# Optimization experiments

Hardware: AMD Instinct MI355X
Metric: run time of the kernel (lower is better)

## Reference

```python
import jax, jax.numpy as jnp
import numpy as np

DIM = 512
NUM_HEADS = 8
HEAD_DIM = DIM // NUM_HEADS


def setup_inputs() -> dict:
    key = jax.random.key(0)
    k1, k2, k3, k4 = jax.random.split(key, 4)
    B, N = 8, 32 * 32
    x = jax.random.normal(k1, (B, N, DIM), dtype=jnp.float32)
    # nn.Linear(dim, 3*dim, bias=False): weight [3*dim, dim], y = x @ W.T
    w_qkv = jax.random.normal(k2, (3 * DIM, DIM), dtype=jnp.float32) * 0.02
    w_proj = jax.random.normal(k3, (DIM, DIM), dtype=jnp.float32) * 0.02
    log_decay = jnp.zeros((NUM_HEADS,), dtype=jnp.float32)
    return {"x": x, "w_qkv": w_qkv, "w_proj": w_proj, "log_decay": log_decay,
            "H": 32, "W": 32}


def _manhattan_dist(H: int, W: int) -> jnp.ndarray:
    # [H*W, H*W] Manhattan distance between grid positions
    rows = jnp.repeat(jnp.arange(H), W)  # [N]
    cols = jnp.tile(jnp.arange(W), H)    # [N]
    dist = (jnp.abs(rows[:, None] - rows[None, :])
            + jnp.abs(cols[:, None] - cols[None, :]))
    return dist.astype(jnp.float32)


def reference(x, w_qkv, w_proj, log_decay, H, W):
    B, N, C = x.shape
    nh, hd = NUM_HEADS, HEAD_DIM
    scale = hd ** -0.5
    qkv = jnp.einsum('bnc,dc->bnd', x, w_qkv)          # [B, N, 3C]
    qkv = qkv.reshape(B, N, 3, nh, hd).transpose(2, 0, 3, 1, 4)
    q, k, v = qkv[0], qkv[1], qkv[2]                   # [B, nh, N, hd]
    attn = jnp.einsum('bhid,bhjd->bhij', q, k) * scale  # [B, nh, N, N]
    dist = _manhattan_dist(H, W)                        # [N, N]
    decay = jax.nn.softplus(log_decay)                  # [nh]
    bias = -decay[:, None, None] * dist[None]           # [nh, N, N]
    attn = jax.nn.softmax(attn + bias[None], axis=-1)
    out = jnp.einsum('bhij,bhjd->bhid', attn, v)        # [B, nh, N, hd]
    out = out.transpose(0, 2, 1, 3).reshape(B, N, C)
    return jnp.einsum('bnc,dc->bnd', out, w_proj)


if __name__ == "__main__":
    out = reference(**setup_inputs())
    print(out.shape, out.dtype)
```

## Files before the change

### kernel.cpp

```cpp
#include <hip/hip_runtime.h>
#include <stdint.h>

typedef _Float16 f16;
typedef _Float16 f16x8 __attribute__((ext_vector_type(8)));
typedef _Float16 f16x4 __attribute__((ext_vector_type(4)));
typedef _Float16 f16x2 __attribute__((ext_vector_type(2)));
typedef float f32x4 __attribute__((ext_vector_type(4)));

#define MROWS 8192
#define KDIM 512
#define NSEQ 1024
#define NH 8

__device__ __forceinline__ void gload16(void* lds, const void* g) {
  __builtin_amdgcn_global_load_lds(
      (const __attribute__((address_space(1))) unsigned*)g,
      (__attribute__((address_space(3))) unsigned*)lds, 16, 0, 0);
}

__device__ __forceinline__ f32x4 mfma16(f16x8 a, f16x8 b, f32x4 c) {
  return __builtin_amdgcn_mfma_f32_16x16x32_f16(a, b, c, 0, 0, 0);
}

__global__ __launch_bounds__(256) void cvt_kernel(
    const float* __restrict__ x, const float* __restrict__ wq,
    const float* __restrict__ wp, f16* __restrict__ x16,
    f16* __restrict__ wq16, f16* __restrict__ wp16) {
  int t = blockIdx.x * 256 + threadIdx.x;
  int stride = gridDim.x * 256;
  for (int i = t; i < (MROWS * KDIM) / 4; i += stride) {
    float4 v = ((const float4*)x)[i];
    f16x4 o = {(f16)v.x, (f16)v.y, (f16)v.z, (f16)v.w};
    ((f16x4*)x16)[i] = o;
  }
  for (int i = t; i < (3 * KDIM * KDIM) / 4; i += stride) {
    float4 v = ((const float4*)wq)[i];
    f16x4 o = {(f16)v.x, (f16)v.y, (f16)v.z, (f16)v.w};
    ((f16x4*)wq16)[i] = o;
  }
  for (int i = t; i < (KDIM * KDIM) / 4; i += stride) {
    float4 v = ((const float4*)wp)[i];
    f16x4 o = {(f16)v.x, (f16)v.y, (f16)v.z, (f16)v.w};
    ((f16x4*)wp16)[i] = o;
  }
}

__device__ __forceinline__ void gemm_mainloop_db(
    const f16* __restrict__ A, const f16* __restrict__ B, int m0, int n0,
    f16* As0, f16* As1, f16* Bs0, f16* Bs1, f32x4 (&acc)[4][4]) {
  const int tid = threadIdx.x;
  const int w = tid >> 6, l = tid & 63;
  const int wr = w >> 1, wc = w & 1;
  const int lrow = l & 15, lk = l >> 4;
  const int srow = l >> 3, sslot = l & 7;
  const int scol = ((sslot ^ srow) << 3);
  const int NT = KDIM / 64;

  auto STAGE = [&](int bb, int kb) {
    f16* Ad = bb ? As1 : As0;
    f16* Bd = bb ? Bs1 : Bs0;
#pragma unroll
    for (int j = 0; j < 4; ++j) {
      int i = w * 4 + j;
      int row = i * 8 + srow;
      gload16(Ad + i * 512, A + (size_t)(m0 + row) * KDIM + kb + scol);
      gload16(Bd + i * 512, B + (size_t)(n0 + row) * KDIM + kb + scol);
    }
  };

  STAGE(0, 0);
#pragma unroll 1
  for (int t = 0; t < NT; ++t) {
    if (t + 1 < NT) {
      STAGE((t + 1) & 1, (t + 1) * 64);
      asm volatile("s_waitcnt vmcnt(8)" ::: "memory");
    } else {
      asm volatile("s_waitcnt vmcnt(0)" ::: "memory");
    }
    __builtin_amdgcn_s_barrier();
    const f16* Asr = (t & 1) ? As1 : As0;
    const f16* Bsr = (t & 1) ? Bs1 : Bs0;
#pragma unroll
    for (int kk = 0; kk < 2; ++kk) {
      int slotbase = kk * 4 + lk;
      f16x8 af[4], bf[4];
#pragma unroll
      for (int mi = 0; mi < 4; ++mi) {
        int row = wr * 64 + mi * 16 + lrow;
        af[mi] = *(const f16x8*)(Asr + row * 64 + ((slotbase ^ (row & 7)) << 3));
      }
#pragma unroll
      for (int nj = 0; nj < 4; ++nj) {
        int row = wc * 64 + nj * 16 + lrow;
        bf[nj] = *(const f16x8*)(Bsr + row * 64 + ((slotbase ^ (row & 7)) << 3));
      }
#pragma unroll
      for (int mi = 0; mi < 4; ++mi)
#pragma unroll
        for (int nj = 0; nj < 4; ++nj)
          acc[mi][nj] = mfma16(af[mi], bf[nj], acc[mi][nj]);
    }
    __builtin_amdgcn_s_barrier();
  }
}

__global__ __launch_bounds__(256, 2) void qkv_gemm(
    const f16* __restrict__ x16, const f16* __restrict__ wq16,
    f16* __restrict__ q16, f16* __restrict__ k16, f16* __restrict__ v16) {
  __shared__ f16 As0[128 * 64], As1[128 * 64];
  __shared__ f16 Bs0[128 * 64], Bs1[128 * 64];
  f32x4 acc[4][4];
#pragma unroll
  for (int i = 0; i < 4; ++i)
#pragma unroll
    for (int j = 0; j < 4; ++j) acc[i][j] = (f32x4){0.f, 0.f, 0.f, 0.f};

  const int m0 = blockIdx.y * 128, n0 = blockIdx.x * 128;
  gemm_mainloop_db(x16, wq16, m0, n0, As0, As1, Bs0, Bs1, acc);

  const int tid = threadIdx.x;
  const int w = tid >> 6, l = tid & 63;
  const int wr = w >> 1, wc = w & 1;
#pragma unroll
  for (int mi = 0; mi < 4; ++mi) {
#pragma unroll
    for (int rr = 0; rr < 4; ++rr) {
      int m = m0 + wr * 64 + mi * 16 + (l >> 4) * 4 + rr;
      int b = m >> 10, n = m & 1023;
#pragma unroll
      for (int nj = 0; nj < 4; ++nj) {
        int d = n0 + wc * 64 + nj * 16 + (l & 15);
        int which = d >> 9, c = d & 511;
        int h = c >> 6, dd = c & 63;
        f16* dst = (which == 0) ? q16 : (which == 1) ? k16 : v16;
        dst[(((size_t)(b * NH + h)) * NSEQ + n) * 64 + dd] = (f16)acc[mi][nj][rr];
      }
    }
  }
}

__global__ __launch_bounds__(256, 2) void proj_gemm(
    const f16* __restrict__ a16, const f16* __restrict__ wp16,
    float* __restrict__ out) {
  __shared__ f16 As0[128 * 64], As1[128 * 64];
  __shared__ f16 Bs0[128 * 64], Bs1[128 * 64];
  f32x4 acc[4][4];
#pragma unroll
  for (int i = 0; i < 4; ++i)
#pragma unroll
    for (int j = 0; j < 4; ++j) acc[i][j] = (f32x4){0.f, 0.f, 0.f, 0.f};

  const int m0 = blockIdx.y * 128, n0 = blockIdx.x * 128;
  gemm_mainloop_db(a16, wp16, m0, n0, As0, As1, Bs0, Bs1, acc);

  const int tid = threadIdx.x;
  const int w = tid >> 6, l = tid & 63;
  const int wr = w >> 1, wc = w & 1;
#pragma unroll
  for (int mi = 0; mi < 4; ++mi) {
#pragma unroll
    for (int rr = 0; rr < 4; ++rr) {
      int m = m0 + wr * 64 + mi * 16 + (l >> 4) * 4 + rr;
#pragma unroll
      for (int nj = 0; nj < 4; ++nj) {
        int d = n0 + wc * 64 + nj * 16 + (l & 15);
        out[(size_t)m * KDIM + d] = acc[mi][nj][rr];
      }
    }
  }
}

__device__ __forceinline__ int swzd(int d) {
  return ((d >> 1) & 3) | ((d & 1) << 2);
}

__global__ __launch_bounds__(256, 2) void attn_f16(
    const f16* __restrict__ q16, const f16* __restrict__ k16,
    const f16* __restrict__ v16, const float* __restrict__ log_decay,
    f16* __restrict__ aout) {
  __shared__ f16 Ks0[64 * 64], Ks1[64 * 64];
  __shared__ f16 Vs0[64 * 64], Vs1[64 * 64];
  __shared__ f16 Vt[64 * 64];
  __shared__ f16 Ps[128 * 64];

  const int tid = threadIdx.x;
  const int w = tid >> 6, l = tid & 63;
  const int lrow = l & 15, lk = l >> 4;
  const int srow = l >> 3, sslot = l & 7;
  const int scol = ((sslot ^ srow) << 3);
  const int q0 = blockIdx.x * 128;
  const int h = blockIdx.y, b = blockIdx.z;
  const size_t base = ((size_t)(b * NH + h)) * NSEQ * 64;

  const float decay = log1pf(__expf(log_decay[h]));

  f16x8 qf[2][2];
#pragma unroll
  for (int njq = 0; njq < 2; ++njq)
#pragma unroll
    for (int kk = 0; kk < 2; ++kk) {
      int row = q0 + w * 32 + njq * 16 + lrow;
      f16x8 v = *(const f16x8*)(q16 + base + (size_t)row * 64 + kk * 32 + lk * 8);
#pragma unroll
      for (int e = 0; e < 8; ++e) v[e] = v[e] * (f16)0.125f;
      qf[njq][kk] = v;
    }

  int qr_[2], qc_[2];
#pragma unroll
  for (int njq = 0; njq < 2; ++njq) {
    int qn = q0 + w * 32 + njq * 16 + lrow;
    qr_[njq] = qn >> 5;
    qc_[njq] = qn & 31;
  }

  f32x4 O[2][4];
#pragma unroll
  for (int njq = 0; njq < 2; ++njq)
#pragma unroll
    for (int dj = 0; dj < 4; ++dj) O[njq][dj] = (f32x4){0.f, 0.f, 0.f, 0.f};
  float mrow[2] = {-1e30f, -1e30f}, lsum[2] = {0.f, 0.f};

  auto STAGE_T = [&](int bb, int c0) {
    f16* Kd = bb ? Ks1 : Ks0;
    f16* Vd = bb ? Vs1 : Vs0;
#pragma unroll
    for (int j = 0; j < 2; ++j) {
      int i = w * 2 + j;
      int row = i * 8 + srow;
      gload16(Kd + i * 512, k16 + base + (size_t)(c0 + row) * 64 + scol);
      gload16(Vd + i * 512, v16 + base + (size_t)(c0 + row) * 64 + (sslot << 3));
    }
  };

  STAGE_T(0, 0);
#pragma unroll 1
  for (int t = 0; t < NSEQ / 64; ++t) {
    const int c0 = t * 64;
    const int cur = t & 1;
    if (t + 1 < NSEQ / 64) {
      STAGE_T(cur ^ 1, c0 + 64);
      asm volatile("s_waitcnt vmcnt(4)" ::: "memory");
    } else {
      asm volatile("s_waitcnt vmcnt(0)" ::: "memory");
    }
    __builtin_amdgcn_s_barrier();

    {
      const f16* vsrc = cur ? Vs1 : Vs0;
      int dd = (tid & 31) * 2;
      int kq = tid >> 5;
      f16x8 v0, v1;
#pragma unroll
      for (int i = 0; i < 8; ++i) {
        f16x2 pr = *(const f16x2*)(vsrc + (size_t)(kq * 8 + i) * 64 + dd);
        v0[i] = pr.x;
        v1[i] = pr.y;
      }
      *(f16x8*)(Vt + (size_t)dd * 64 + ((kq ^ swzd(dd)) << 3)) = v0;
      *(f16x8*)(Vt + (size_t)(dd + 1) * 64 + ((kq ^ swzd(dd + 1)) << 3)) = v1;
    }

    const f16* ksrc = cur ? Ks1 : Ks0;
    f32x4 s[4][2];
#pragma unroll
    for (int mi = 0; mi < 4; ++mi)
#pragma unroll
      for (int njq = 0; njq < 2; ++njq) s[mi][njq] = (f32x4){0.f, 0.f, 0.f, 0.f};
#pragma unroll
    for (int kk = 0; kk < 2; ++kk) {
      int slotbase = kk * 4 + lk;
#pragma unroll
      for (int mi = 0; mi < 4; ++mi) {
        int row = mi * 16 + lrow;
        f16x8 kf = *(const f16x8*)(ksrc + row * 64 + ((slotbase ^ (row & 7)) << 3));
#pragma unroll
        for (int njq = 0; njq < 2; ++njq)
          s[mi][njq] = mfma16(kf, qf[njq][kk], s[mi][njq]);
      }
    }

    float al[2];
#pragma unroll
    for (int njq = 0; njq < 2; ++njq) {
      float mx = -1e30f;
#pragma unroll
      for (int mi = 0; mi < 4; ++mi) {
        int kvb = c0 + mi * 16 + lk * 4;
        int krb = kvb >> 5, kcb = kvb & 31;
        float dr = (float)__builtin_abs(qr_[njq] - krb);
        int t1 = qc_[njq] - kcb;
#pragma unroll
        for (int rr = 0; rr < 4; ++rr) {
          float dc = (float)__builtin_abs(t1 - rr);
          float tt = fmaf(-decay, dr + dc, s[mi][njq][rr]);
          s[mi][njq][rr] = tt;
          mx = fmaxf(mx, tt);
        }
      }
      mx = fmaxf(mx, __shfl_xor(mx, 16));
      mx = fmaxf(mx, __shfl_xor(mx, 32));
      float mnew = fmaxf(mrow[njq], mx);
      al[njq] = __expf(mrow[njq] - mnew);
      mrow[njq] = mnew;
      float rs = 0.f;
      int qq = w * 32 + njq * 16 + lrow;
#pragma unroll
      for (int mi = 0; mi < 4; ++mi) {
        f16x4 pw;
#pragma unroll
        for (int rr = 0; rr < 4; ++rr) {
          float p = __expf(s[mi][njq][rr] - mnew);
          rs += p;
          pw[rr] = (f16)p;
        }
        int slot = mi * 2 + (lk >> 1);
        *(f16x4*)(Ps + qq * 64 + ((slot ^ (qq & 7)) << 3) + ((lk & 1) << 2)) = pw;
      }
      rs += __shfl_xor(rs, 16);
      rs += __shfl_xor(rs, 32);
      lsum[njq] = lsum[njq] * al[njq] + rs;
    }

#pragma unroll
    for (int njq = 0; njq < 2; ++njq) {
#pragma unroll
      for (int rr = 0; rr < 4; ++rr) {
        float a = __shfl(al[njq], lk * 4 + rr);
#pragma unroll
        for (int dj = 0; dj < 4; ++dj) O[njq][dj][rr] *= a;
      }
    }

    asm volatile("s_waitcnt lgkmcnt(0)" ::: "memory");
    __builtin_amdgcn_s_barrier();

#pragma unroll
    for (int kk = 0; kk < 2; ++kk) {
      int slotbase = kk * 4 + lk;
      f16x8 pa[2], vb[4];
#pragma unroll
      for (int njq = 0; njq < 2; ++njq) {
        int row = w * 32 + njq * 16 + lrow;
        pa[njq] = *(const f16x8*)(Ps + row * 64 + ((slotbase ^ (row & 7)) << 3));
      }
#pragma unroll
      for (int dj = 0; dj < 4; ++dj) {
        int d = dj * 16 + lrow;
        vb[dj] = *(const f16x8*)(Vt + d * 64 + ((slotbase ^ swzd(d)) << 3));
      }
#pragma unroll
      for (int njq = 0; njq < 2; ++njq)
#pragma unroll
        for (int dj = 0; dj < 4; ++dj)
          O[njq][dj] = mfma16(pa[njq], vb[dj], O[njq][dj]);
    }
  }

  float linv[2] = {1.f / lsum[0], 1.f / lsum[1]};
#pragma unroll
  for (int njq = 0; njq < 2; ++njq) {
#pragma unroll
    for (int rr = 0; rr < 4; ++rr) {
      float inv = __shfl(linv[njq], lk * 4 + rr);
      int qn = q0 + w * 32 + njq * 16 + lk * 4 + rr;
      size_t rowbase = ((size_t)(b * NSEQ + qn)) * KDIM + h * 64;
#pragma unroll
      for (int dj = 0; dj < 4; ++dj)
        aout[rowbase + dj * 16 + lrow] = (f16)(O[njq][dj][rr] * inv);
    }
  }
}

extern "C" void kernel_launch(void* const* d_in, const int* in_sizes, int n_in,
                              void* d_out, int out_size, void* d_ws, size_t ws_size,
                              hipStream_t stream) {
  const float* x = (const float*)d_in[0];
  const float* w_qkv = (const float*)d_in[1];
  const float* w_proj = (const float*)d_in[2];
  const float* log_decay = (const float*)d_in[3];

  f16* ws = (f16*)d_ws;
  f16* x16 = ws;
  f16* wq16 = x16 + (size_t)MROWS * KDIM;
  f16* wp16 = wq16 + (size_t)3 * KDIM * KDIM;
  f16* q16 = wp16 + (size_t)KDIM * KDIM;
  f16* k16 = q16 + (size_t)MROWS * KDIM;
  f16* v16 = k16 + (size_t)MROWS * KDIM;
  f16* a16 = v16 + (size_t)MROWS * KDIM;

  cvt_kernel<<<1024, 256, 0, stream>>>(x, w_qkv, w_proj, x16, wq16, wp16);
  qkv_gemm<<<dim3(12, 64), 256, 0, stream>>>(x16, wq16, q16, k16, v16);
  attn_f16<<<dim3(8, NH, 8), 256, 0, stream>>>(q16, k16, v16, log_decay, a16);
  proj_gemm<<<dim3(4, 64), 256, 0, stream>>>(a16, wp16, (float*)d_out);
}
```

Before: 155.8 us.

## Store V transposed from QKV GEMM and pass P through registers in attention

The QKV GEMM now writes V in a transposed [head, dim, seq] layout, so the attention kernel loads V tiles straight into LDS already transposed and no longer transposes them per tile. Softmax probabilities are packed to f16 and redistributed into the MFMA A-operand layout with cross-lane shuffles instead of going through an LDS P buffer. The attention block tile shrinks to 64 queries (one 16-row slice per wave) and the grid doubles, with launch bounds raised to 4 blocks per CU. The goals are less LDS traffic, fewer barriers and higher occupancy. The cost is strided scalar stores of V in the GEMM epilogue and extra shuffle instructions per tile.

```diff
diff --git a/kernel.cpp b/kernel.cpp
--- a/kernel.cpp
+++ b/kernel.cpp
@@ -20,6 +20,10 @@
 
 __device__ __forceinline__ f32x4 mfma16(f16x8 a, f16x8 b, f32x4 c) {
   return __builtin_amdgcn_mfma_f32_16x16x32_f16(a, b, c, 0, 0, 0);
+}
+
+__device__ __forceinline__ int vsg(int d) {
+  return ((d >> 1) & 7) ^ ((d & 1) << 2);
 }
 
 __global__ __launch_bounds__(256) void cvt_kernel(
@@ -106,7 +110,7 @@
 
 __global__ __launch_bounds__(256, 2) void qkv_gemm(
     const f16* __restrict__ x16, const f16* __restrict__ wq16,
-    f16* __restrict__ q16, f16* __restrict__ k16, f16* __restrict__ v16) {
+    f16* __restrict__ q16, f16* __restrict__ k16, f16* __restrict__ v16T) {
   __shared__ f16 As0[128 * 64], As1[128 * 64];
   __shared__ f16 Bs0[128 * 64], Bs1[128 * 64];
   f32x4 acc[4][4];
@@ -132,8 +136,14 @@
         int d = n0 + wc * 64 + nj * 16 + (l & 15);
         int which = d >> 9, c = d & 511;
         int h = c >> 6, dd = c & 63;
-        f16* dst = (which == 0) ? q16 : (which == 1) ? k16 : v16;
-        dst[(((size_t)(b * NH + h)) * NSEQ + n) * 64 + dd] = (f16)acc[mi][nj][rr];
+        f16 val = (f16)acc[mi][nj][rr];
+        size_t hb = (size_t)(b * NH + h);
+        if (which == 0)
+          q16[(hb * NSEQ + n) * 64 + dd] = val;
+        else if (which == 1)
+          k16[(hb * NSEQ + n) * 64 + dd] = val;
+        else
+          v16T[(hb * 64 + dd) * NSEQ + n] = val;
       }
     }
   }
@@ -170,205 +180,173 @@
   }
 }
 
-__device__ __forceinline__ int swzd(int d) {
-  return ((d >> 1) & 3) | ((d & 1) << 2);
-}
-
-__global__ __launch_bounds__(256, 2) void attn_f16(
+__global__ __launch_bounds__(256, 4) void attn_f16(
     const f16* __restrict__ q16, const f16* __restrict__ k16,
-    const f16* __restrict__ v16, const float* __restrict__ log_decay,
+    const f16* __restrict__ v16T, const float* __restrict__ log_decay,
     f16* __restrict__ aout) {
   __shared__ f16 Ks0[64 * 64], Ks1[64 * 64];
-  __shared__ f16 Vs0[64 * 64], Vs1[64 * 64];
-  __shared__ f16 Vt[64 * 64];
-  __shared__ f16 Ps[128 * 64];
+  __shared__ f16 Vt0[64 * 64], Vt1[64 * 64];
 
   const int tid = threadIdx.x;
   const int w = tid >> 6, l = tid & 63;
   const int lrow = l & 15, lk = l >> 4;
   const int srow = l >> 3, sslot = l & 7;
-  const int scol = ((sslot ^ srow) << 3);
-  const int q0 = blockIdx.x * 128;
+  const int q0 = blockIdx.x * 64;
   const int h = blockIdx.y, b = blockIdx.z;
-  const size_t base = ((size_t)(b * NH + h)) * NSEQ * 64;
+  const size_t kbase = ((size_t)(b * NH + h)) * NSEQ * 64;
+  const size_t vbase = ((size_t)(b * NH + h)) * 64 * NSEQ;
 
   const float decay = log1pf(__expf(log_decay[h]));
 
-  f16x8 qf[2][2];
-#pragma unroll
-  for (int njq = 0; njq < 2; ++njq)
-#pragma unroll
-    for (int kk = 0; kk < 2; ++kk) {
-      int row = q0 + w * 32 + njq * 16 + lrow;
-      f16x8 v = *(const f16x8*)(q16 + base + (size_t)row * 64 + kk * 32 + lk * 8);
-#pragma unroll
-      for (int e = 0; e < 8; ++e) v[e] = v[e] * (f16)0.125f;
-      qf[njq][kk] = v;
-    }
-
-  int qr_[2], qc_[2];
-#pragma unroll
-  for (int njq = 0; njq < 2; ++njq) {
-    int qn = q0 + w * 32 + njq * 16 + lrow;
-    qr_[njq] = qn >> 5;
-    qc_[njq] = qn & 31;
-  }
-
-  f32x4 O[2][4];
-#pragma unroll
-  for (int njq = 0; njq < 2; ++njq)
-#pragma unroll
-    for (int dj = 0; dj < 4; ++dj) O[njq][dj] = (f32x4){0.f, 0.f, 0.f, 0.f};
-  float mrow[2] = {-1e30f, -1e30f}, lsum[2] = {0.f, 0.f};
-
-  auto STAGE_T = [&](int bb, int c0) {
+  f16x8 qf[2];
+#pragma unroll
+  for (int kk = 0; kk < 2; ++kk) {
+    int row = q0 + w * 16 + lrow;
+    f16x8 v = *(const f16x8*)(q16 + kbase + (size_t)row * 64 + kk * 32 + lk * 8);
+#pragma unroll
+    for (int e = 0; e < 8; ++e) v[e] = v[e] * (f16)0.125f;
+    qf[kk] = v;
+  }
+
+  const int qn = q0 + w * 16 + lrow;
+  const int qr = qn >> 5, qc = qn & 31;
+
+  f32x4 O[4];
+#pragma unroll
+  for (int dj = 0; dj < 4; ++dj) O[dj] = (f32x4){0.f, 0.f, 0.f, 0.f};
+  float mrow = -1e30f, lsum = 0.f;
+
+  auto STAGE = [&](int bb, int c0) {
     f16* Kd = bb ? Ks1 : Ks0;
-    f16* Vd = bb ? Vs1 : Vs0;
+    f16* Vd = bb ? Vt1 : Vt0;
 #pragma unroll
     for (int j = 0; j < 2; ++j) {
       int i = w * 2 + j;
-      int row = i * 8 + srow;
-      gload16(Kd + i * 512, k16 + base + (size_t)(c0 + row) * 64 + scol);
-      gload16(Vd + i * 512, v16 + base + (size_t)(c0 + row) * 64 + (sslot << 3));
+      int krow = i * 8 + srow;
+      gload16(Kd + i * 512,
+              k16 + kbase + (size_t)(c0 + krow) * 64 + ((sslot ^ (krow & 7)) << 3));
+      int d = i * 8 + srow;
+      gload16(Vd + i * 512,
+              v16T + vbase + (size_t)d * NSEQ + c0 + ((sslot ^ vsg(d)) << 3));
     }
   };
 
-  STAGE_T(0, 0);
+  const int srcA = lrow + ((l >> 4) & 1) * 32;
+  const int srcB = srcA + 16;
+  const int msel = lk >> 1;
+
+  STAGE(0, 0);
 #pragma unroll 1
   for (int t = 0; t < NSEQ / 64; ++t) {
     const int c0 = t * 64;
     const int cur = t & 1;
+    __builtin_amdgcn_s_barrier();
     if (t + 1 < NSEQ / 64) {
-      STAGE_T(cur ^ 1, c0 + 64);
+      STAGE(cur ^ 1, c0 + 64);
       asm volatile("s_waitcnt vmcnt(4)" ::: "memory");
     } else {
       asm volatile("s_waitcnt vmcnt(0)" ::: "memory");
     }
     __builtin_amdgcn_s_barrier();
-
-    {
-      const f16* vsrc = cur ? Vs1 : Vs0;
-      int dd = (tid & 31) * 2;
-      int kq = tid >> 5;
-      f16x8 v0, v1;
-#pragma unroll
-      for (int i = 0; i < 8; ++i) {
-        f16x2 pr = *(const f16x2*)(vsrc + (size_t)(kq * 8 + i) * 64 + dd);
-        v0[i] = pr.x;
-        v1[i] = pr.y;
-      }
-      *(f16x8*)(Vt + (size_t)dd * 64 + ((kq ^ swzd(dd)) << 3)) = v0;
-      *(f16x8*)(Vt + (size_t)(dd + 1) * 64 + ((kq ^ swzd(dd + 1)) << 3)) = v1;
-    }
-
-    const f16* ksrc = cur ? Ks1 : Ks0;
-    f32x4 s[4][2];
-#pragma unroll
-    for (int mi = 0; mi < 4; ++mi)
-#pragma unroll
-      for (int njq = 0; njq < 2; ++njq) s[mi][njq] = (f32x4){0.f, 0.f, 0.f, 0.f};
+    const f16* Kc = cur ? Ks1 : Ks0;
+    const f16* Vc = cur ? Vt1 : Vt0;
+
+    f32x4 s[4];
+#pragma unroll
+    for (int mi = 0; mi < 4; ++mi) s[mi] = (f32x4){0.f, 0.f, 0.f, 0.f};
 #pragma unroll
     for (int kk = 0; kk < 2; ++kk) {
-      int slotbase = kk * 4 + lk;
 #pragma unroll
       for (int mi = 0; mi < 4; ++mi) {
         int row = mi * 16 + lrow;
-        f16x8 kf = *(const f16x8*)(ksrc + row * 64 + ((slotbase ^ (row & 7)) << 3));
-#pragma unroll
-        for (int njq = 0; njq < 2; ++njq)
-          s[mi][njq] = mfma16(kf, qf[njq][kk], s[mi][njq]);
-      }
-    }
-
-    float al[2];
-#pragma unroll
-    for (int njq = 0; njq < 2; ++njq) {
-      float mx = -1e30f;
-#pragma unroll
-      for (int mi = 0; mi < 4; ++mi) {
-        int kvb = c0 + mi * 16 + lk * 4;
-        int krb = kvb >> 5, kcb = kvb & 31;
-        float dr = (float)__builtin_abs(qr_[njq] - krb);
-        int t1 = qc_[njq] - kcb;
-#pragma unroll
-        for (int rr = 0; rr < 4; ++rr) {
-          float dc = (float)__builtin_abs(t1 - rr);
-          float tt = fmaf(-decay, dr + dc, s[mi][njq][rr]);
-          s[mi][njq][rr] = tt;
-          mx = fmaxf(mx, tt);
-        }
-      }
-      mx = fmaxf(mx, __shfl_xor(mx, 16));
-      mx = fmaxf(mx, __shfl_xor(mx, 32));
-      float mnew = fmaxf(mrow[njq], mx);
-      al[njq] = __expf(mrow[njq] - mnew);
-      mrow[njq] = mnew;
-      float rs = 0.f;
-      int qq = w * 32 + njq * 16 + lrow;
-#pragma unroll
-      for (int mi = 0; mi < 4; ++mi) {
-        f16x4 pw;
-#pragma unroll
-        for (int rr = 0; rr < 4; ++rr) {
-          float p = __expf(s[mi][njq][rr] - mnew);
-          rs += p;
-          pw[rr] = (f16)p;
-        }
-        int slot = mi * 2 + (lk >> 1);
-        *(f16x4*)(Ps + qq * 64 + ((slot ^ (qq & 7)) << 3) + ((lk & 1) << 2)) = pw;
-      }
-      rs += __shfl_xor(rs, 16);
-      rs += __shfl_xor(rs, 32);
-      lsum[njq] = lsum[njq] * al[njq] + rs;
-    }
-
-#pragma unroll
-    for (int njq = 0; njq < 2; ++njq) {
+        f16x8 kf = *(const f16x8*)(Kc + row * 64 + (((kk * 4 + lk) ^ (row & 7)) << 3));
+        s[mi] = mfma16(kf, qf[kk], s[mi]);
+      }
+    }
+
+    float mx = -1e30f;
+#pragma unroll
+    for (int mi = 0; mi < 4; ++mi) {
+      int kvb = c0 + mi * 16 + lk * 4;
+      int krb = kvb >> 5, kcb = kvb & 31;
+      float dr = (float)__builtin_abs(qr - krb);
+      int t1 = qc - kcb;
 #pragma unroll
       for (int rr = 0; rr < 4; ++rr) {
-        float a = __shfl(al[njq], lk * 4 + rr);
-#pragma unroll
-        for (int dj = 0; dj < 4; ++dj) O[njq][dj][rr] *= a;
-      }
-    }
-
-    asm volatile("s_waitcnt lgkmcnt(0)" ::: "memory");
-    __builtin_amdgcn_s_barrier();
+        float dc = (float)__builtin_abs(t1 - rr);
+        float tt = fmaf(-decay, dr + dc, s[mi][rr]);
+        s[mi][rr] = tt;
+        mx = fmaxf(mx, tt);
+      }
+    }
+    mx = fmaxf(mx, __shfl_xor(mx, 16));
+    mx = fmaxf(mx, __shfl_xor(mx, 32));
+    float mnew = fmaxf(mrow, mx);
+    float al = __expf(mrow - mnew);
+    mrow = mnew;
+    float rs = 0.f;
+    unsigned wpk[4][2];
+#pragma unroll
+    for (int mi = 0; mi < 4; ++mi) {
+#pragma unroll
+      for (int j = 0; j < 2; ++j) {
+        float p0 = __expf(s[mi][2 * j] - mnew);
+        float p1 = __expf(s[mi][2 * j + 1] - mnew);
+        rs += p0 + p1;
+        union { f16x2 h; unsigned u; } pk;
+        pk.h = (f16x2){(f16)p0, (f16)p1};
+        wpk[mi][j] = pk.u;
+      }
+    }
+    rs += __shfl_xor(rs, 16);
+    rs += __shfl_xor(rs, 32);
+    lsum = lsum * al + rs;
+
+#pragma unroll
+    for (int rr = 0; rr < 4; ++rr) {
+      float a = __shfl(al, lk * 4 + rr);
+#pragma unroll
+      for (int dj = 0; dj < 4; ++dj) O[dj][rr] *= a;
+    }
 
 #pragma unroll
     for (int kk = 0; kk < 2; ++kk) {
-      int slotbase = kk * 4 + lk;
-      f16x8 pa[2], vb[4];
-#pragma unroll
-      for (int njq = 0; njq < 2; ++njq) {
-        int row = w * 32 + njq * 16 + lrow;
-        pa[njq] = *(const f16x8*)(Ps + row * 64 + ((slotbase ^ (row & 7)) << 3));
-      }
+      unsigned paw[4];
+      {
+        int a0 = __shfl((int)wpk[kk * 2][0], srcA);
+        int b0 = __shfl((int)wpk[kk * 2 + 1][0], srcA);
+        paw[0] = (unsigned)(msel ? b0 : a0);
+        int a1 = __shfl((int)wpk[kk * 2][1], srcA);
+        int b1 = __shfl((int)wpk[kk * 2 + 1][1], srcA);
+        paw[1] = (unsigned)(msel ? b1 : a1);
+        int a2 = __shfl((int)wpk[kk * 2][0], srcB);
+        int b2 = __shfl((int)wpk[kk * 2 + 1][0], srcB);
+        paw[2] = (unsigned)(msel ? b2 : a2);
+        int a3 = __shfl((int)wpk[kk * 2][1], srcB);
+        int b3 = __shfl((int)wpk[kk * 2 + 1][1], srcB);
+        paw[3] = (unsigned)(msel ? b3 : a3);
+      }
+      union { unsigned u[4]; f16x8 v; } pc;
+      pc.u[0] = paw[0]; pc.u[1] = paw[1]; pc.u[2] = paw[2]; pc.u[3] = paw[3];
+      f16x8 pa = pc.v;
 #pragma unroll
       for (int dj = 0; dj < 4; ++dj) {
         int d = dj * 16 + lrow;
-        vb[dj] = *(const f16x8*)(Vt + d * 64 + ((slotbase ^ swzd(d)) << 3));
-      }
-#pragma unroll
-      for (int njq = 0; njq < 2; ++njq)
-#pragma unroll
-        for (int dj = 0; dj < 4; ++dj)
-          O[njq][dj] = mfma16(pa[njq], vb[dj], O[njq][dj]);
-    }
-  }
-
-  float linv[2] = {1.f / lsum[0], 1.f / lsum[1]};
-#pragma unroll
-  for (int njq = 0; njq < 2; ++njq) {
-#pragma unroll
-    for (int rr = 0; rr < 4; ++rr) {
-      float inv = __shfl(linv[njq], lk * 4 + rr);
-      int qn = q0 + w * 32 + njq * 16 + lk * 4 + rr;
-      size_t rowbase = ((size_t)(b * NSEQ + qn)) * KDIM + h * 64;
-#pragma unroll
-      for (int dj = 0; dj < 4; ++dj)
-        aout[rowbase + dj * 16 + lrow] = (f16)(O[njq][dj][rr] * inv);
-    }
+        f16x8 vb = *(const f16x8*)(Vc + d * 64 + (((kk * 4 + lk) ^ vsg(d)) << 3));
+        O[dj] = mfma16(pa, vb, O[dj]);
+      }
+    }
+  }
+
+  float linv = 1.f / lsum;
+#pragma unroll
+  for (int rr = 0; rr < 4; ++rr) {
+    float inv = __shfl(linv, lk * 4 + rr);
+    int q = q0 + w * 16 + lk * 4 + rr;
+    size_t rowbase = ((size_t)(b * NSEQ + q)) * KDIM + h * 64;
+#pragma unroll
+    for (int dj = 0; dj < 4; ++dj)
+      aout[rowbase + dj * 16 + lrow] = (f16)(O[dj][rr] * inv);
   }
 }
 
@@ -386,11 +364,11 @@
   f16* wp16 = wq16 + (size_t)3 * KDIM * KDIM;
   f16* q16 = wp16 + (size_t)KDIM * KDIM;
   f16* k16 = q16 + (size_t)MROWS * KDIM;
-  f16* v16 = k16 + (size_t)MROWS * KDIM;
-  f16* a16 = v16 + (size_t)MROWS * KDIM;
+  f16* v16T = k16 + (size_t)MROWS * KDIM;
+  f16* a16 = v16T + (size_t)MROWS * KDIM;
 
   cvt_kernel<<<1024, 256, 0, stream>>>(x, w_qkv, w_proj, x16, wq16, wp16);
-  qkv_gemm<<<dim3(12, 64), 256, 0, stream>>>(x16, wq16, q16, k16, v16);
-  attn_f16<<<dim3(8, NH, 8), 256, 0, stream>>>(q16, k16, v16, log_decay, a16);
+  qkv_gemm<<<dim3(12, 64), 256, 0, stream>>>(x16, wq16, q16, k16, v16T);
+  attn_f16<<<dim3(16, NH, 8), 256, 0, stream>>>(q16, k16, v16T, log_decay, a16);
   proj_gemm<<<dim3(4, 64), 256, 0, stream>>>(a16, wp16, (float*)d_out);
 }
```

Result: slower. 172.9 us (+10.9%).

## Emit V transposed from QKV GEMM and double-buffer P in attention

Applied to the files above, without the earlier changes.

The QKV GEMM epilogue now writes V in a head-dim-major transposed layout, staged through shared memory so the stores are coalesced. The attention kernel can then load V^T straight into swizzled LDS instead of transposing it in every tile. Attention also double-buffers the P tile, precomputes the column part of the Manhattan bias per lane, and remaps the grid so blocks for the same (batch, head) are spread out. The prefetch moves to after the barrier and waits vmcnt(0), which may expose more load latency in exchange for removing the per-tile transpose and a barrier hazard.

```diff
diff --git a/kernel.cpp b/kernel.cpp
--- a/kernel.cpp
+++ b/kernel.cpp
@@ -4,7 +4,6 @@
 typedef _Float16 f16;
 typedef _Float16 f16x8 __attribute__((ext_vector_type(8)));
 typedef _Float16 f16x4 __attribute__((ext_vector_type(4)));
-typedef _Float16 f16x2 __attribute__((ext_vector_type(2)));
 typedef float f32x4 __attribute__((ext_vector_type(4)));
 
 #define MROWS 8192
@@ -20,6 +19,10 @@
 
 __device__ __forceinline__ f32x4 mfma16(f16x8 a, f16x8 b, f32x4 c) {
   return __builtin_amdgcn_mfma_f32_16x16x32_f16(a, b, c, 0, 0, 0);
+}
+
+__device__ __forceinline__ int vsg(int d) {
+  return ((d >> 1) & 7) ^ ((d & 1) << 2);
 }
 
 __global__ __launch_bounds__(256) void cvt_kernel(
@@ -106,9 +109,13 @@
 
 __global__ __launch_bounds__(256, 2) void qkv_gemm(
     const f16* __restrict__ x16, const f16* __restrict__ wq16,
-    f16* __restrict__ q16, f16* __restrict__ k16, f16* __restrict__ v16) {
-  __shared__ f16 As0[128 * 64], As1[128 * 64];
-  __shared__ f16 Bs0[128 * 64], Bs1[128 * 64];
+    f16* __restrict__ q16, f16* __restrict__ k16, f16* __restrict__ v16T) {
+  __shared__ f16 SMEM[4 * 128 * 64];
+  f16* As0 = SMEM;
+  f16* As1 = SMEM + 8192;
+  f16* Bs0 = SMEM + 16384;
+  f16* Bs1 = SMEM + 24576;
+
   f32x4 acc[4][4];
 #pragma unroll
   for (int i = 0; i < 4; ++i)
@@ -121,20 +128,54 @@
   const int tid = threadIdx.x;
   const int w = tid >> 6, l = tid & 63;
   const int wr = w >> 1, wc = w & 1;
-#pragma unroll
-  for (int mi = 0; mi < 4; ++mi) {
-#pragma unroll
-    for (int rr = 0; rr < 4; ++rr) {
-      int m = m0 + wr * 64 + mi * 16 + (l >> 4) * 4 + rr;
-      int b = m >> 10, n = m & 1023;
+  const int lrow = l & 15, lk = l >> 4;
+
+  if (n0 < 1024) {
+#pragma unroll
+    for (int mi = 0; mi < 4; ++mi) {
+#pragma unroll
+      for (int rr = 0; rr < 4; ++rr) {
+        int m = m0 + wr * 64 + mi * 16 + lk * 4 + rr;
+        int b = m >> 10, n = m & 1023;
+#pragma unroll
+        for (int nj = 0; nj < 4; ++nj) {
+          int d = n0 + wc * 64 + nj * 16 + lrow;
+          int which = d >> 9, c = d & 511;
+          int h = c >> 6, dd = c & 63;
+          f16 val = (f16)acc[mi][nj][rr];
+          size_t hb = (size_t)(b * NH + h);
+          if (which == 0)
+            q16[(hb * NSEQ + n) * 64 + dd] = val;
+          else
+            k16[(hb * NSEQ + n) * 64 + dd] = val;
+        }
+      }
+    }
+  } else {
+    f16* T = SMEM;
+#pragma unroll
+    for (int mi = 0; mi < 4; ++mi) {
 #pragma unroll
       for (int nj = 0; nj < 4; ++nj) {
-        int d = n0 + wc * 64 + nj * 16 + (l & 15);
-        int which = d >> 9, c = d & 511;
-        int h = c >> 6, dd = c & 63;
-        f16* dst = (which == 0) ? q16 : (which == 1) ? k16 : v16;
-        dst[(((size_t)(b * NH + h)) * NSEQ + n) * 64 + dd] = (f16)acc[mi][nj][rr];
-      }
+        int dloc = wc * 64 + nj * 16 + lrow;
+        int nloc = wr * 64 + mi * 16 + lk * 4;
+        f16x4 pw = {(f16)acc[mi][nj][0], (f16)acc[mi][nj][1],
+                    (f16)acc[mi][nj][2], (f16)acc[mi][nj][3]};
+        *(f16x4*)(T + dloc * 136 + nloc) = pw;
+      }
+    }
+    __syncthreads();
+    const int b = m0 >> 10;
+    const int nbase = m0 & 1023;
+#pragma unroll
+    for (int rs = 0; rs < 8; ++rs) {
+      int dloc = w * 32 + rs * 4 + (l >> 4);
+      int ncol = (l & 15) * 8;
+      f16x8 vv = *(const f16x8*)(T + dloc * 136 + ncol);
+      int c = (n0 + dloc) & 511;
+      int hh = c >> 6, dd = c & 63;
+      size_t hb = (size_t)(b * NH + hh);
+      *(f16x8*)(v16T + (hb * 64 + dd) * NSEQ + nbase + ncol) = vv;
     }
   }
 }
@@ -170,29 +211,29 @@
   }
 }
 
-__device__ __forceinline__ int swzd(int d) {
-  return ((d >> 1) & 3) | ((d & 1) << 2);
-}
-
 __global__ __launch_bounds__(256, 2) void attn_f16(
     const f16* __restrict__ q16, const f16* __restrict__ k16,
-    const f16* __restrict__ v16, const float* __restrict__ log_decay,
+    const f16* __restrict__ v16T, const float* __restrict__ log_decay,
     f16* __restrict__ aout) {
   __shared__ f16 Ks0[64 * 64], Ks1[64 * 64];
-  __shared__ f16 Vs0[64 * 64], Vs1[64 * 64];
-  __shared__ f16 Vt[64 * 64];
-  __shared__ f16 Ps[128 * 64];
+  __shared__ f16 Vt0[64 * 64], Vt1[64 * 64];
+  __shared__ f16 Ps0[128 * 64], Ps1[128 * 64];
 
   const int tid = threadIdx.x;
   const int w = tid >> 6, l = tid & 63;
   const int lrow = l & 15, lk = l >> 4;
   const int srow = l >> 3, sslot = l & 7;
-  const int scol = ((sslot ^ srow) << 3);
-  const int q0 = blockIdx.x * 128;
-  const int h = blockIdx.y, b = blockIdx.z;
-  const size_t base = ((size_t)(b * NH + h)) * NSEQ * 64;
+
+  const int L = blockIdx.x;
+  const int pair = (L & 7) * 8 + ((L >> 3) & 7);
+  const int q0 = (L >> 6) * 128;
+  const int b = pair >> 3, h = pair & 7;
+
+  const size_t kbase = ((size_t)(b * NH + h)) * NSEQ * 64;
+  const size_t vbase = ((size_t)(b * NH + h)) * 64 * NSEQ;
 
   const float decay = log1pf(__expf(log_decay[h]));
+  const float negdecay = -decay;
 
   f16x8 qf[2][2];
 #pragma unroll
@@ -200,7 +241,7 @@
 #pragma unroll
     for (int kk = 0; kk < 2; ++kk) {
       int row = q0 + w * 32 + njq * 16 + lrow;
-      f16x8 v = *(const f16x8*)(q16 + base + (size_t)row * 64 + kk * 32 + lk * 8);
+      f16x8 v = *(const f16x8*)(q16 + kbase + (size_t)row * 64 + kk * 32 + lk * 8);
 #pragma unroll
       for (int e = 0; e < 8; ++e) v[e] = v[e] * (f16)0.125f;
       qf[njq][kk] = v;
@@ -214,6 +255,19 @@
     qc_[njq] = qn & 31;
   }
 
+  float bdc[2][4][4];
+#pragma unroll
+  for (int njq = 0; njq < 2; ++njq)
+#pragma unroll
+    for (int mi = 0; mi < 4; ++mi)
+#pragma unroll
+      for (int rr = 0; rr < 4; ++rr) {
+        int kc = (mi * 16 + lk * 4 + rr) & 31;
+        int da = qc_[njq] - kc;
+        da = (da < 0) ? -da : da;
+        bdc[njq][mi][rr] = negdecay * (float)da;
+      }
+
   f32x4 O[2][4];
 #pragma unroll
   for (int njq = 0; njq < 2; ++njq)
@@ -221,47 +275,33 @@
     for (int dj = 0; dj < 4; ++dj) O[njq][dj] = (f32x4){0.f, 0.f, 0.f, 0.f};
   float mrow[2] = {-1e30f, -1e30f}, lsum[2] = {0.f, 0.f};
 
-  auto STAGE_T = [&](int bb, int c0) {
+  auto STAGE = [&](int bb, int cc0) {
     f16* Kd = bb ? Ks1 : Ks0;
-    f16* Vd = bb ? Vs1 : Vs0;
+    f16* Vd = bb ? Vt1 : Vt0;
 #pragma unroll
     for (int j = 0; j < 2; ++j) {
       int i = w * 2 + j;
       int row = i * 8 + srow;
-      gload16(Kd + i * 512, k16 + base + (size_t)(c0 + row) * 64 + scol);
-      gload16(Vd + i * 512, v16 + base + (size_t)(c0 + row) * 64 + (sslot << 3));
+      gload16(Kd + i * 512,
+              k16 + kbase + (size_t)(cc0 + row) * 64 + ((sslot ^ (row & 7)) << 3));
+      gload16(Vd + i * 512,
+              v16T + vbase + (size_t)row * NSEQ + cc0 + ((sslot ^ vsg(row)) << 3));
     }
   };
 
-  STAGE_T(0, 0);
+  STAGE(0, 0);
 #pragma unroll 1
   for (int t = 0; t < NSEQ / 64; ++t) {
     const int c0 = t * 64;
     const int cur = t & 1;
-    if (t + 1 < NSEQ / 64) {
-      STAGE_T(cur ^ 1, c0 + 64);
-      asm volatile("s_waitcnt vmcnt(4)" ::: "memory");
-    } else {
-      asm volatile("s_waitcnt vmcnt(0)" ::: "memory");
-    }
+    asm volatile("s_waitcnt vmcnt(0)" ::: "memory");
     __builtin_amdgcn_s_barrier();
-
-    {
-      const f16* vsrc = cur ? Vs1 : Vs0;
-      int dd = (tid & 31) * 2;
-      int kq = tid >> 5;
-      f16x8 v0, v1;
-#pragma unroll
-      for (int i = 0; i < 8; ++i) {
-        f16x2 pr = *(const f16x2*)(vsrc + (size_t)(kq * 8 + i) * 64 + dd);
-        v0[i] = pr.x;
-        v1[i] = pr.y;
-      }
-      *(f16x8*)(Vt + (size_t)dd * 64 + ((kq ^ swzd(dd)) << 3)) = v0;
-      *(f16x8*)(Vt + (size_t)(dd + 1) * 64 + ((kq ^ swzd(dd + 1)) << 3)) = v1;
-    }
-
-    const f16* ksrc = cur ? Ks1 : Ks0;
+    if (t + 1 < NSEQ / 64) STAGE(cur ^ 1, c0 + 64);
+
+    const f16* Kc = cur ? Ks1 : Ks0;
+    const f16* Vc = cur ? Vt1 : Vt0;
+    f16* Psc = cur ? Ps1 : Ps0;
+
     f32x4 s[4][2];
 #pragma unroll
     for (int mi = 0; mi < 4; ++mi)
@@ -269,31 +309,37 @@
       for (int njq = 0; njq < 2; ++njq) s[mi][njq] = (f32x4){0.f, 0.f, 0.f, 0.f};
 #pragma unroll
     for (int kk = 0; kk < 2; ++kk) {
-      int slotbase = kk * 4 + lk;
 #pragma unroll
       for (int mi = 0; mi < 4; ++mi) {
         int row = mi * 16 + lrow;
-        f16x8 kf = *(const f16x8*)(ksrc + row * 64 + ((slotbase ^ (row & 7)) << 3));
+        f16x8 kf = *(const f16x8*)(Kc + row * 64 + (((kk * 4 + lk) ^ (row & 7)) << 3));
 #pragma unroll
         for (int njq = 0; njq < 2; ++njq)
           s[mi][njq] = mfma16(kf, qf[njq][kk], s[mi][njq]);
       }
     }
 
+    float bdr[2][2];
+#pragma unroll
+    for (int njq = 0; njq < 2; ++njq) {
+      int d0 = qr_[njq] - 2 * t;
+      int a0 = (d0 < 0) ? -d0 : d0;
+      int d1 = d0 - 1;
+      int a1 = (d1 < 0) ? -d1 : d1;
+      bdr[njq][0] = negdecay * (float)a0;
+      bdr[njq][1] = negdecay * (float)a1;
+    }
+
     float al[2];
 #pragma unroll
     for (int njq = 0; njq < 2; ++njq) {
       float mx = -1e30f;
 #pragma unroll
       for (int mi = 0; mi < 4; ++mi) {
-        int kvb = c0 + mi * 16 + lk * 4;
-        int krb = kvb >> 5, kcb = kvb & 31;
-        float dr = (float)__builtin_abs(qr_[njq] - krb);
-        int t1 = qc_[njq] - kcb;
+        float bdrm = bdr[njq][mi >> 1];
 #pragma unroll
         for (int rr = 0; rr < 4; ++rr) {
-          float dc = (float)__builtin_abs(t1 - rr);
-          float tt = fmaf(-decay, dr + dc, s[mi][njq][rr]);
+          float tt = s[mi][njq][rr] + (bdc[njq][mi][rr] + bdrm);
           s[mi][njq][rr] = tt;
           mx = fmaxf(mx, tt);
         }
@@ -315,7 +361,7 @@
           pw[rr] = (f16)p;
         }
         int slot = mi * 2 + (lk >> 1);
-        *(f16x4*)(Ps + qq * 64 + ((slot ^ (qq & 7)) << 3) + ((lk & 1) << 2)) = pw;
+        *(f16x4*)(Psc + qq * 64 + ((slot ^ (qq & 7)) << 3) + ((lk & 1) << 2)) = pw;
       }
       rs += __shfl_xor(rs, 16);
       rs += __shfl_xor(rs, 32);
@@ -342,12 +388,12 @@
 #pragma unroll
       for (int njq = 0; njq < 2; ++njq) {
         int row = w * 32 + njq * 16 + lrow;
-        pa[njq] = *(const f16x8*)(Ps + row * 64 + ((slotbase ^ (row & 7)) << 3));
+        pa[njq] = *(const f16x8*)(Psc + row * 64 + ((slotbase ^ (row & 7)) << 3));
       }
 #pragma unroll
       for (int dj = 0; dj < 4; ++dj) {
         int d = dj * 16 + lrow;
-        vb[dj] = *(const f16x8*)(Vt + d * 64 + ((slotbase ^ swzd(d)) << 3));
+        vb[dj] = *(const f16x8*)(Vc + d * 64 + ((slotbase ^ vsg(d)) << 3));
       }
 #pragma unroll
       for (int njq = 0; njq < 2; ++njq)
@@ -386,11 +432,11 @@
   f16* wp16 = wq16 + (size_t)3 * KDIM * KDIM;
   f16* q16 = wp16 + (size_t)KDIM * KDIM;
   f16* k16 = q16 + (size_t)MROWS * KDIM;
-  f16* v16 = k16 + (size_t)MROWS * KDIM;
-  f16* a16 = v16 + (size_t)MROWS * KDIM;
+  f16* v16T = k16 + (size_t)MROWS * KDIM;
+  f16* a16 = v16T + (size_t)MROWS * KDIM;
 
   cvt_kernel<<<1024, 256, 0, stream>>>(x, w_qkv, w_proj, x16, wq16, wp16);
-  qkv_gemm<<<dim3(12, 64), 256, 0, stream>>>(x16, wq16, q16, k16, v16);
-  attn_f16<<<dim3(8, NH, 8), 256, 0, stream>>>(q16, k16, v16, log_decay, a16);
+  qkv_gemm<<<dim3(12, 64), 256, 0, stream>>>(x16, wq16, q16, k16, v16T);
+  attn_f16<<<dim3(512), 256, 0, stream>>>(q16, k16, v16T, log_decay, a16);
   proj_gemm<<<dim3(4, 64), 256, 0, stream>>>(a16, wp16, (float*)d_out);
 }
```

Measured after the change: 146.4 us. 1.06x faster.
